# Performance work log

Hardware: AMD Instinct MI355X
Metric: run time of the kernel (lower is better)

## Reference

```python
import jax, jax.numpy as jnp
import numpy as np

HIDDEN = 2048
NUM_Q_HEADS = 16
NUM_KV_HEADS = 4
HEAD_DIM = HIDDEN // NUM_Q_HEADS  # 128
KV_REP = NUM_Q_HEADS // NUM_KV_HEADS  # 4
KV_DIM = HEAD_DIM * NUM_KV_HEADS


def setup_inputs() -> dict:
    key = jax.random.key(0)
    ks = jax.random.split(key, 9)
    B, S = 2, 2048
    s_in = 1.0 / np.sqrt(HIDDEN)
    return {
        "hidden_states": jax.random.normal(ks[0], (B, S, HIDDEN), dtype=jnp.float32),
        "Wq": jax.random.normal(ks[1], (HIDDEN, HIDDEN), dtype=jnp.float32) * s_in,
        "bq": jnp.zeros((HIDDEN,), dtype=jnp.float32),
        "Wk": jax.random.normal(ks[2], (HIDDEN, KV_DIM), dtype=jnp.float32) * s_in,
        "bk": jnp.zeros((KV_DIM,), dtype=jnp.float32),
        "Wv": jax.random.normal(ks[3], (HIDDEN, KV_DIM), dtype=jnp.float32) * s_in,
        "bv": jnp.zeros((KV_DIM,), dtype=jnp.float32),
        "Wo": jax.random.normal(ks[4], (HIDDEN, HIDDEN), dtype=jnp.float32) * s_in,
        "bo": jnp.zeros((HIDDEN,), dtype=jnp.float32),
    }


def reference(hidden_states, Wq, bq, Wk, bk, Wv, bv, Wo, bo):
    B, S, H = hidden_states.shape
    # projections
    q = hidden_states @ Wq + bq  # [B,S,H]
    k = hidden_states @ Wk + bk  # [B,S,KV_DIM]
    v = hidden_states @ Wv + bv  # [B,S,KV_DIM]
    # [B, heads, S, head_dim]
    q = q.reshape(B, S, NUM_Q_HEADS, HEAD_DIM).transpose(0, 2, 1, 3)
    k = k.reshape(B, S, NUM_KV_HEADS, HEAD_DIM).transpose(0, 2, 1, 3)
    v = v.reshape(B, S, NUM_KV_HEADS, HEAD_DIM).transpose(0, 2, 1, 3)
    # repeat_interleave KV heads to match q heads
    k = jnp.repeat(k, KV_REP, axis=1)  # [B,Hq,S,hd]
    v = jnp.repeat(v, KV_REP, axis=1)
    scale = 1.0 / np.sqrt(HEAD_DIM)
    scores = jnp.einsum('bhqd,bhkd->bhqk', q, k) * scale  # [B,Hq,S,S]
    causal = jnp.triu(jnp.ones((S, S), dtype=bool), k=1)
    scores = jnp.where(causal[None, None], -jnp.inf, scores)
    probs = jax.nn.softmax(scores, axis=-1)
    ctx = jnp.einsum('bhqk,bhkd->bhqd', probs, v)  # [B,Hq,S,hd]
    ctx = ctx.transpose(0, 2, 1, 3).reshape(B, S, H)
    return ctx @ Wo + bo
```

## Files before the change

### kernel.cpp

```cpp
#include <hip/hip_runtime.h>
#include <hip/hip_bf16.h>
#include <stdint.h>

#define SEQ 2048
#define BATCH 2
#define NTOK (SEQ * BATCH)
#define HID 2048
#define NQH 16
#define NKVH 4
#define HD 128
#define KVD 512

typedef __bf16 bf16x8 __attribute__((ext_vector_type(8)));
typedef float f32x4 __attribute__((ext_vector_type(4)));
typedef float f32x16 __attribute__((ext_vector_type(16)));
typedef unsigned int u32;

__device__ __forceinline__ unsigned short f2bf(float f) {
    uint32_t u = __builtin_bit_cast(uint32_t, f);
    uint32_t r = (u + 0x7fffu + ((u >> 16) & 1u)) >> 16;
    return (unsigned short)r;
}

__device__ __forceinline__ u32 cvtpk(float lo, float hi) {
    u32 r;
    asm("v_cvt_pk_bf16_f32 %0, %1, %2" : "=v"(r) : "v"(lo), "v"(hi));
    return r;
}

__device__ __forceinline__ void gload16(const void* g, void* l) {
    __builtin_amdgcn_global_load_lds((const __attribute__((address_space(1))) u32*)g,
                                     (__attribute__((address_space(3))) u32*)l, 16, 0, 0);
}

__global__ void cvt_f32_bf16(const float* __restrict__ in, unsigned short* __restrict__ out, int n4) {
    int i = blockIdx.x * blockDim.x + threadIdx.x;
    int stride = gridDim.x * blockDim.x;
    for (; i < n4; i += stride) {
        float4 v = ((const float4*)in)[i];
        ushort4 o;
        o.x = f2bf(v.x); o.y = f2bf(v.y); o.z = f2bf(v.z); o.w = f2bf(v.w);
        ((ushort4*)out)[i] = o;
    }
}

__global__ __launch_bounds__(256) void transpose_all(const float* __restrict__ Wq,
                                                     const float* __restrict__ Wk,
                                                     const float* __restrict__ Wv,
                                                     const float* __restrict__ Wo,
                                                     unsigned short* __restrict__ Wqkvt,
                                                     unsigned short* __restrict__ Wot) {
    __shared__ unsigned short tile[64][72];
    const int y = blockIdx.y;
    const float* W;
    unsigned short* dst;
    int N, ny;
    if (y < 32)      { W = Wq; dst = Wqkvt;                        N = 2048; ny = y; }
    else if (y < 40) { W = Wk; dst = Wqkvt + (size_t)2048 * HID;   N = 512;  ny = y - 32; }
    else if (y < 48) { W = Wv; dst = Wqkvt + (size_t)2560 * HID;   N = 512;  ny = y - 40; }
    else             { W = Wo; dst = Wot;                          N = 2048; ny = y - 48; }
    const int k0 = blockIdx.x * 64, n0 = ny * 64;
    const int t = threadIdx.x;
    const int r = t >> 4;
    const int c4 = (t & 15) * 4;
    #pragma unroll
    for (int i = 0; i < 4; i++) {
        int row = r + i * 16;
        float4 v = *(const float4*)&W[(size_t)(k0 + row) * N + n0 + c4];
        tile[row][c4 + 0] = f2bf(v.x);
        tile[row][c4 + 1] = f2bf(v.y);
        tile[row][c4 + 2] = f2bf(v.z);
        tile[row][c4 + 3] = f2bf(v.w);
    }
    __syncthreads();
    #pragma unroll
    for (int i = 0; i < 4; i++) {
        int nrow = r + i * 16;
        ushort4 o;
        o.x = tile[c4 + 0][nrow];
        o.y = tile[c4 + 1][nrow];
        o.z = tile[c4 + 2][nrow];
        o.w = tile[c4 + 3][nrow];
        *(ushort4*)&dst[(size_t)(n0 + nrow) * HID + k0 + c4] = o;
    }
}

template <int MODE>
__global__ __launch_bounds__(256) void gemm128(const unsigned short* __restrict__ A,
                                               const unsigned short* __restrict__ Bt,
                                               const float* __restrict__ b0,
                                               const float* __restrict__ b1,
                                               const float* __restrict__ b2,
                                               void* __restrict__ o0,
                                               void* __restrict__ o1,
                                               void* __restrict__ o2) {
    __shared__ __align__(16) unsigned short Asm[2][128 * 32];
    __shared__ __align__(16) unsigned short Bsm[2][128 * 32];
    const int m0 = blockIdx.x * 128;
    const int nb = blockIdx.y;
    const int n0 = nb * 128;
    const int t = threadIdx.x;
    const int lane = t & 63, w = t >> 6;
    const int wr = (w >> 1) * 64, wc = (w & 1) * 64;
    const int l16 = lane & 15, lg = lane >> 4;

    f32x4 acc[4][4] = {};

    auto stage = [&](int buf, int kt) {
        const int k0 = kt * 32;
        #pragma unroll
        for (int j = 0; j < 2; j++) {
            int c = j * 256 + t;
            int row = c >> 2, s = c & 3;
            int cg = s ^ ((row >> 1) & 3);
            char* dA = (char*)&Asm[buf][0] + (j * 256 + w * 64) * 16;
            char* dB = (char*)&Bsm[buf][0] + (j * 256 + w * 64) * 16;
            gload16(&A[(size_t)(m0 + row) * HID + k0 + cg * 8], dA);
            gload16(&Bt[(size_t)(n0 + row) * HID + k0 + cg * 8], dB);
        }
    };

    stage(0, 0);
    __syncthreads();
    int buf = 0;
    for (int kt = 0; kt < HID / 32; kt++) {
        if (kt < HID / 32 - 1) stage(buf ^ 1, kt + 1);
        const char* Ab = (const char*)&Asm[buf][0];
        const char* Bb = (const char*)&Bsm[buf][0];
        bf16x8 af[4], bfr[4];
        #pragma unroll
        for (int m = 0; m < 4; m++) {
            int row = wr + m * 16 + l16;
            af[m] = *(const bf16x8*)(Ab + row * 64 + ((lg ^ ((row >> 1) & 3)) << 4));
        }
        #pragma unroll
        for (int n = 0; n < 4; n++) {
            int row = wc + n * 16 + l16;
            bfr[n] = *(const bf16x8*)(Bb + row * 64 + ((lg ^ ((row >> 1) & 3)) << 4));
        }
        #pragma unroll
        for (int m = 0; m < 4; m++)
            #pragma unroll
            for (int n = 0; n < 4; n++)
                acc[m][n] = __builtin_amdgcn_mfma_f32_16x16x32_bf16(af[m], bfr[n], acc[m][n], 0, 0, 0);
        __syncthreads();
        buf ^= 1;
    }

    const float sc = 0.08838834764831845f;
    #pragma unroll
    for (int m = 0; m < 4; m++) {
        int row = m0 + wr + m * 16 + lg * 4;
        #pragma unroll
        for (int n = 0; n < 4; n++) {
            int col = n0 + wc + n * 16 + l16;
            #pragma unroll
            for (int r = 0; r < 4; r++) {
                float v = acc[m][n][r];
                int rr = row + r;
                if constexpr (MODE == 0) {
                    if (nb < 16) {
                        v = (v + b0[col]) * sc;
                        ((unsigned short*)o0)[(size_t)rr * HID + col] = f2bf(v);
                    } else if (nb < 20) {
                        int c = col - 2048;
                        v += b1[c];
                        ((unsigned short*)o1)[(size_t)rr * KVD + c] = f2bf(v);
                    } else {
                        int c = col - 2560;
                        v += b2[c];
                        int b = rr >> 11, s = rr & (SEQ - 1);
                        ((unsigned short*)o2)[((size_t)b * KVD + c) * SEQ + s] = f2bf(v);
                    }
                } else {
                    v += b0[col];
                    ((float*)o0)[(size_t)rr * HID + col] = v;
                }
            }
        }
    }
}

__global__ __launch_bounds__(256, 2) void attn(const unsigned short* __restrict__ Q,
                                               const unsigned short* __restrict__ K,
                                               const unsigned short* __restrict__ Vt,
                                               unsigned short* __restrict__ ctx) {
    __shared__ unsigned short Ksm[2][64 * 128];
    __shared__ unsigned short Vsm[2][128 * 64];
    const int n = blockIdx.x;
    const int qt = 15 - (n >> 5);
    const int bh = n & 31;
    const int b = bh >> 4, h = bh & 15, hk = h >> 2;
    const int t = threadIdx.x, w = t >> 6, lane = t & 63;
    const int lam = lane & 31, hi = lane >> 5;
    const int qw = qt * 128 + w * 32;
    const int qg = qw + lam;
    const size_t qrowbase = (size_t)b * SEQ + qw;

    const unsigned short* Kg = K + (size_t)b * SEQ * KVD + hk * HD;
    const unsigned short* Vg = Vt + ((size_t)b * KVD + hk * HD) * SEQ;

    bf16x8 qf[8];
    #pragma unroll
    for (int kc = 0; kc < 8; kc++)
        qf[kc] = *(const bf16x8*)&Q[(qrowbase + lam) * HID + h * HD + kc * 16 + hi * 8];

    f32x16 oacc[4] = {};
    float m = -1e30f, l = 0.f;

    auto stage = [&](int buf, int kt) {
        const int kvb = kt * 64;
        #pragma unroll
        for (int it = 0; it < 4; it++) {
            int base = it * 256 + w * 64;
            int qc = base + lane;
            {
                int row = qc >> 4, c = qc & 15;
                gload16(&Kg[(size_t)(kvb + row) * KVD + ((c ^ (row & 7)) << 3)],
                        (char*)&Ksm[buf][0] + base * 16);
            }
            {
                int row = qc >> 3, c = qc & 7;
                gload16(&Vg[(size_t)row * SEQ + kvb + ((c ^ (row & 7)) << 3)],
                        (char*)&Vsm[buf][0] + base * 16);
            }
        }
    };

    const int ntile = 2 * qt + 2;
    stage(0, 0);
    __syncthreads();
    int buf = 0;
    for (int kt = 0; kt < ntile; kt++) {
        const int kvb = kt * 64;
        if (kt + 1 < ntile) stage(buf ^ 1, kt + 1);
        if (kvb <= qw + 31) {
            const char* Kb = (const char*)&Ksm[buf][0];
            const char* Vb = (const char*)&Vsm[buf][0];
            f32x16 st0 = {}, st1 = {};
            #pragma unroll
            for (int kc = 0; kc < 8; kc++) {
                int coff = (kc * 32 + hi * 16) ^ ((lam & 7) << 4);
                bf16x8 kf0 = *(const bf16x8*)(Kb + lam * 256 + coff);
                bf16x8 kf1 = *(const bf16x8*)(Kb + (32 + lam) * 256 + coff);
                st0 = __builtin_amdgcn_mfma_f32_32x32x16_bf16(kf0, qf[kc], st0, 0, 0, 0);
                st1 = __builtin_amdgcn_mfma_f32_32x32x16_bf16(kf1, qf[kc], st1, 0, 0, 0);
            }
            if (kvb + 63 > qw) {
                #pragma unroll
                for (int r = 0; r < 16; r++) {
                    int krow = (r & 3) + 8 * (r >> 2) + 4 * hi;
                    if (kvb + krow > qg) st0[r] = -1e30f;
                    if (kvb + 32 + krow > qg) st1[r] = -1e30f;
                }
            }
            float tmax = st0[0];
            #pragma unroll
            for (int r = 1; r < 16; r++) tmax = fmaxf(tmax, st0[r]);
            #pragma unroll
            for (int r = 0; r < 16; r++) tmax = fmaxf(tmax, st1[r]);
            tmax = fmaxf(tmax, __shfl_xor(tmax, 32));
            float mn = fmaxf(m, tmax);
            float sf = __expf(m - mn);
            m = mn;
            float rs = 0.f;
            #pragma unroll
            for (int r = 0; r < 16; r++) { st0[r] = __expf(st0[r] - mn); rs += st0[r]; }
            #pragma unroll
            for (int r = 0; r < 16; r++) { st1[r] = __expf(st1[r] - mn); rs += st1[r]; }
            rs += __shfl_xor(rs, 32);
            l = l * sf + rs;
            #pragma unroll
            for (int dc = 0; dc < 4; dc++)
                #pragma unroll
                for (int r = 0; r < 16; r++) oacc[dc][r] *= sf;
            u32 pw0[4][2], pw1[4][2];
            #pragma unroll
            for (int g = 0; g < 4; g++) {
                pw0[g][0] = cvtpk(st0[4 * g], st0[4 * g + 1]);
                pw0[g][1] = cvtpk(st0[4 * g + 2], st0[4 * g + 3]);
                pw1[g][0] = cvtpk(st1[4 * g], st1[4 * g + 1]);
                pw1[g][1] = cvtpk(st1[4 * g + 2], st1[4 * g + 3]);
            }
            #pragma unroll
            for (int kc = 0; kc < 4; kc++) {
                const u32 (*pw)[2] = (kc >> 1) ? pw1 : pw0;
                int g0 = (kc & 1) * 2;
                u32 own0 = hi ? pw[g0 + 1][0] : pw[g0][0];
                u32 own1 = hi ? pw[g0 + 1][1] : pw[g0][1];
                u32 off0 = hi ? pw[g0][0] : pw[g0 + 1][0];
                u32 off1 = hi ? pw[g0][1] : pw[g0 + 1][1];
                u32 xw0 = __shfl_xor(off0, 32);
                u32 xw1 = __shfl_xor(off1, 32);
                int4 paw;
                paw.x = hi ? xw0 : own0;
                paw.y = hi ? xw1 : own1;
                paw.z = hi ? own0 : xw0;
                paw.w = hi ? own1 : xw1;
                bf16x8 pa = __builtin_bit_cast(bf16x8, paw);
                #pragma unroll
                for (int dc = 0; dc < 4; dc++) {
                    bf16x8 vf = *(const bf16x8*)(Vb + (dc * 32 + lam) * 128 +
                                                 ((kc * 32 + hi * 16) ^ ((lam & 7) << 4)));
                    oacc[dc] = __builtin_amdgcn_mfma_f32_32x32x16_bf16(vf, pa, oacc[dc], 0, 0, 0);
                }
            }
        }
        __syncthreads();
        buf ^= 1;
    }

    float inv = 1.f / l;
    char* osm = (char*)&Ksm[0][0] + w * 8192;
    #pragma unroll
    for (int dc = 0; dc < 4; dc++)
        #pragma unroll
        for (int r = 0; r < 16; r += 2) {
            int d = dc * 32 + (r & 3) + 8 * (r >> 2) + 4 * hi;
            u32 wd = cvtpk(oacc[dc][r] * inv, oacc[dc][r + 1] * inv);
            *(u32*)(osm + lam * 256 + ((d * 2) ^ ((lam & 7) << 4))) = wd;
        }
    __syncthreads();
    const int q2 = lane >> 1, half = lane & 1;
    #pragma unroll
    for (int cc = 0; cc < 8; cc++) {
        bf16x8 v = *(const bf16x8*)(osm + q2 * 256 + (((half * 8 + cc) * 16) ^ ((q2 & 7) << 4)));
        *(bf16x8*)&ctx[(qrowbase + q2) * HID + h * HD + half * 64 + cc * 8] = v;
    }
}

extern "C" void kernel_launch(void* const* d_in, const int* in_sizes, int n_in,
                              void* d_out, int out_size, void* d_ws, size_t ws_size,
                              hipStream_t stream) {
    const float* X  = (const float*)d_in[0];
    const float* Wq = (const float*)d_in[1];
    const float* bq = (const float*)d_in[2];
    const float* Wk = (const float*)d_in[3];
    const float* bk = (const float*)d_in[4];
    const float* Wv = (const float*)d_in[5];
    const float* bv = (const float*)d_in[6];
    const float* Wo = (const float*)d_in[7];
    const float* bo = (const float*)d_in[8];
    float* out = (float*)d_out;

    const size_t MB = 1u << 20;
    char* ws = (char*)d_ws;
    if (ws_size < 76 * MB) return;
    unsigned short* Xb    = (unsigned short*)(ws + 0 * MB);
    unsigned short* Wqkvt = (unsigned short*)(ws + 16 * MB);
    unsigned short* Wot   = (unsigned short*)(ws + 28 * MB);
    unsigned short* Qb    = (unsigned short*)(ws + 36 * MB);
    unsigned short* Kb    = (unsigned short*)(ws + 52 * MB);
    unsigned short* Vtb   = (unsigned short*)(ws + 56 * MB);
    unsigned short* Ctx   = (unsigned short*)(ws + 60 * MB);

    cvt_f32_bf16<<<2048, 256, 0, stream>>>(X, Xb, NTOK * HID / 4);
    transpose_all<<<dim3(32, 80), 256, 0, stream>>>(Wq, Wk, Wv, Wo, Wqkvt, Wot);

    gemm128<0><<<dim3(32, 24), 256, 0, stream>>>(Xb, Wqkvt, bq, bk, bv, Qb, Kb, Vtb);

    attn<<<dim3(512), 256, 0, stream>>>(Qb, Kb, Vtb, Ctx);

    gemm128<1><<<dim3(32, 16), 256, 0, stream>>>(Ctx, Wot, bo, nullptr, nullptr, (void*)out, nullptr, nullptr);
}
```

Before: 219.5 us.

## Single-buffer V, raise attention occupancy, use exp2 softmax with lazy rescale

Folds log2(e) into the Q scale so softmax can use the native exp2 instruction. The online softmax now skips rescaling the output accumulator unless the running max grows by more than a threshold. V is single-buffered and loaded at the start of each tile so the load overlaps QK^T and softmax, with explicit vmcnt waits and barriers. The freed LDS lets launch bounds allow three blocks per CU. The risks are register pressure at the higher occupancy, exposed V load latency, and correctness depending on the hand-written waitcnt ordering.

```diff
diff --git a/kernel.cpp b/kernel.cpp
--- a/kernel.cpp
+++ b/kernel.cpp
@@ -147,7 +147,7 @@
         buf ^= 1;
     }
 
-    const float sc = 0.08838834764831845f;
+    const float sc = 0.12751744954313278f;
     #pragma unroll
     for (int m = 0; m < 4; m++) {
         int row = m0 + wr + m * 16 + lg * 4;
@@ -181,12 +181,12 @@
     }
 }
 
-__global__ __launch_bounds__(256, 2) void attn(const unsigned short* __restrict__ Q,
+__global__ __launch_bounds__(256, 3) void attn(const unsigned short* __restrict__ Q,
                                                const unsigned short* __restrict__ K,
                                                const unsigned short* __restrict__ Vt,
                                                unsigned short* __restrict__ ctx) {
     __shared__ unsigned short Ksm[2][64 * 128];
-    __shared__ unsigned short Vsm[2][128 * 64];
+    __shared__ unsigned short Vsm[128 * 64];
     const int n = blockIdx.x;
     const int qt = 15 - (n >> 5);
     const int bh = n & 31;
@@ -208,35 +208,42 @@
     f32x16 oacc[4] = {};
     float m = -1e30f, l = 0.f;
 
-    auto stage = [&](int buf, int kt) {
+    auto stageK = [&](int buf, int kt) {
         const int kvb = kt * 64;
         #pragma unroll
         for (int it = 0; it < 4; it++) {
             int base = it * 256 + w * 64;
             int qc = base + lane;
-            {
-                int row = qc >> 4, c = qc & 15;
-                gload16(&Kg[(size_t)(kvb + row) * KVD + ((c ^ (row & 7)) << 3)],
-                        (char*)&Ksm[buf][0] + base * 16);
-            }
-            {
-                int row = qc >> 3, c = qc & 7;
-                gload16(&Vg[(size_t)row * SEQ + kvb + ((c ^ (row & 7)) << 3)],
-                        (char*)&Vsm[buf][0] + base * 16);
-            }
+            int row = qc >> 4, c = qc & 15;
+            gload16(&Kg[(size_t)(kvb + row) * KVD + ((c ^ (row & 7)) << 3)],
+                    (char*)&Ksm[buf][0] + base * 16);
         }
     };
+    auto stageV = [&](int kt) {
+        const int kvb = kt * 64;
+        #pragma unroll
+        for (int it = 0; it < 4; it++) {
+            int base = it * 256 + w * 64;
+            int qc = base + lane;
+            int row = qc >> 3, c = qc & 7;
+            gload16(&Vg[(size_t)row * SEQ + kvb + ((c ^ (row & 7)) << 3)],
+                    (char*)&Vsm[0] + base * 16);
+        }
+    };
 
     const int ntile = 2 * qt + 2;
-    stage(0, 0);
+    stageK(0, 0);
+    asm volatile("s_waitcnt vmcnt(0)" ::: "memory");
     __syncthreads();
     int buf = 0;
     for (int kt = 0; kt < ntile; kt++) {
         const int kvb = kt * 64;
-        if (kt + 1 < ntile) stage(buf ^ 1, kt + 1);
-        if (kvb <= qw + 31) {
+        const bool act = (kvb <= qw + 31);
+        stageV(kt);
+        if (kt + 1 < ntile) stageK(buf ^ 1, kt + 1);
+        u32 pw0[4][2], pw1[4][2];
+        if (act) {
             const char* Kb = (const char*)&Ksm[buf][0];
-            const char* Vb = (const char*)&Vsm[buf][0];
             f32x16 st0 = {}, st1 = {};
             #pragma unroll
             for (int kc = 0; kc < 8; kc++) {
@@ -254,27 +261,32 @@
                     if (kvb + 32 + krow > qg) st1[r] = -1e30f;
                 }
             }
-            float tmax = st0[0];
-            #pragma unroll
-            for (int r = 1; r < 16; r++) tmax = fmaxf(tmax, st0[r]);
-            #pragma unroll
-            for (int r = 0; r < 16; r++) tmax = fmaxf(tmax, st1[r]);
+            float mx[8];
+            #pragma unroll
+            for (int r = 0; r < 8; r++) mx[r] = fmaxf(st0[r], st0[r + 8]);
+            #pragma unroll
+            for (int r = 0; r < 8; r++) mx[r] = fmaxf(mx[r], fmaxf(st1[r], st1[r + 8]));
+            #pragma unroll
+            for (int r = 0; r < 4; r++) mx[r] = fmaxf(mx[r], mx[r + 4]);
+            float tmax = fmaxf(fmaxf(mx[0], mx[1]), fmaxf(mx[2], mx[3]));
             tmax = fmaxf(tmax, __shfl_xor(tmax, 32));
-            float mn = fmaxf(m, tmax);
-            float sf = __expf(m - mn);
-            m = mn;
+            if (!__all(tmax - m <= 11.5f)) {
+                float mn = fmaxf(m, tmax);
+                float sf = __builtin_amdgcn_exp2f(m - mn);
+                m = mn;
+                l *= sf;
+                #pragma unroll
+                for (int dc = 0; dc < 4; dc++)
+                    #pragma unroll
+                    for (int r = 0; r < 16; r++) oacc[dc][r] *= sf;
+            }
             float rs = 0.f;
             #pragma unroll
-            for (int r = 0; r < 16; r++) { st0[r] = __expf(st0[r] - mn); rs += st0[r]; }
-            #pragma unroll
-            for (int r = 0; r < 16; r++) { st1[r] = __expf(st1[r] - mn); rs += st1[r]; }
+            for (int r = 0; r < 16; r++) { st0[r] = __builtin_amdgcn_exp2f(st0[r] - m); rs += st0[r]; }
+            #pragma unroll
+            for (int r = 0; r < 16; r++) { st1[r] = __builtin_amdgcn_exp2f(st1[r] - m); rs += st1[r]; }
             rs += __shfl_xor(rs, 32);
-            l = l * sf + rs;
-            #pragma unroll
-            for (int dc = 0; dc < 4; dc++)
-                #pragma unroll
-                for (int r = 0; r < 16; r++) oacc[dc][r] *= sf;
-            u32 pw0[4][2], pw1[4][2];
+            l += rs;
             #pragma unroll
             for (int g = 0; g < 4; g++) {
                 pw0[g][0] = cvtpk(st0[4 * g], st0[4 * g + 1]);
@@ -282,6 +294,12 @@
                 pw1[g][0] = cvtpk(st1[4 * g], st1[4 * g + 1]);
                 pw1[g][1] = cvtpk(st1[4 * g + 2], st1[4 * g + 3]);
             }
+        }
+        if (kt + 1 < ntile) { asm volatile("s_waitcnt vmcnt(4)" ::: "memory"); }
+        else                { asm volatile("s_waitcnt vmcnt(0)" ::: "memory"); }
+        asm volatile("s_barrier" ::: "memory");
+        if (act) {
+            const char* Vb = (const char*)&Vsm[0];
             #pragma unroll
             for (int kc = 0; kc < 4; kc++) {
                 const u32 (*pw)[2] = (kc >> 1) ? pw1 : pw0;
@@ -306,7 +324,8 @@
                 }
             }
         }
-        __syncthreads();
+        asm volatile("s_waitcnt vmcnt(0)" ::: "memory");
+        asm volatile("s_barrier" ::: "memory");
         buf ^= 1;
     }
 
```

Measured after the change: 269.4 us. +22.7%, slower.
